# Kernel optimization log

Hardware: AMD Instinct MI355X
Metric: run time of the kernel (lower is better)

## Reference

```python
import jax, jax.numpy as jnp
import numpy as np

N = 50000      # nodes
E = 800000     # edges (avg degree 16)
IN = 128       # input feature dim
HID = 32       # per-head hidden dim
H = 4          # attention heads
C = 40         # num classes
SLOPE = 0.2    # leaky relu negative slope


def setup_inputs() -> dict:
    key = jax.random.key(0)
    ks = jax.random.split(key, 14)
    s = 0.05
    inputs = jax.random.normal(ks[0], (N, IN), jnp.float32)
    target = jax.random.normal(ks[1], (N, IN), jnp.float32)
    lamb = jax.random.uniform(ks[2], (1,), jnp.float32)
    src = jax.random.randint(ks[3], (E,), 0, N, jnp.int32)
    dst = jax.random.randint(ks[4], (E,), 0, N, jnp.int32)
    W0 = jax.random.normal(ks[5], (IN, H * HID), jnp.float32) * s
    al0 = jax.random.normal(ks[6], (H, HID), jnp.float32) * s
    ar0 = jax.random.normal(ks[7], (H, HID), jnp.float32) * s
    W1 = jax.random.normal(ks[8], (H * HID, H * HID), jnp.float32) * s
    al1 = jax.random.normal(ks[9], (H, HID), jnp.float32) * s
    ar1 = jax.random.normal(ks[10], (H, HID), jnp.float32) * s
    Wout = jax.random.normal(ks[11], (H * HID, C), jnp.float32) * s
    bout = jnp.zeros((C,), jnp.float32)
    return dict(inputs=inputs, target=target, lamb=lamb,
                W0=W0, al0=al0, ar0=ar0, W1=W1, al1=al1, ar1=ar1,
                Wout=Wout, bout=bout, src=src, dst=dst)


def gat_conv(h, W, al, ar, src, dst, residual):
    # h: [N, in_dim]; W: [in_dim, H*HID]; al/ar: [H, HID]
    feat = (h @ W).reshape(N, H, HID)                  # [N,H,D]
    el = jnp.einsum('nhd,hd->nh', feat, al)            # [N,H]
    er = jnp.einsum('nhd,hd->nh', feat, ar)            # [N,H]
    e = jax.nn.leaky_relu(el[src] + er[dst], SLOPE)    # [E,H]
    # edge softmax over incoming edges of each dst node
    emax = jax.ops.segment_max(e, dst, num_segments=N)  # [N,H]
    ee = jnp.exp(e - emax[dst])                          # [E,H]
    denom = jax.ops.segment_sum(ee, dst, num_segments=N)
    a = ee / denom[dst]                                  # [E,H]
    msg = feat[src] * a[:, :, None]                      # [E,H,D]
    out = jax.ops.segment_sum(msg, dst, num_segments=N)  # [N,H,D]
    if residual:
        out = out + h.reshape(N, H, HID)  # identity residual (in == H*HID)
    return jax.nn.elu(out)


def reference(inputs, target, lamb, W0, al0, ar0, W1, al1, ar1, Wout, bout, src, dst):
    def path(x):
        h = gat_conv(x, W0, al0, ar0, src, dst, residual=False).reshape(N, H * HID)
        h = gat_conv(h, W1, al1, ar1, src, dst, residual=True).reshape(N, H * HID)
        return h

    h = path(inputs)
    h2 = path(target)
    lam = lamb[0]
    h = lam * h + (1.0 - lam) * h2   # mixup_hidden=True
    logits = h @ Wout + bout
    return (h, logits)
```

## Files before the change

### kernel.cpp

```cpp
#include <hip/hip_runtime.h>
#include <hip/hip_bf16.h>
#include <cstddef>

#define GN 50000
#define GE 800000
#define GH 4
#define GD 32
#define SLOPE 0.2f
#define LOG2E 1.4426950408889634f

typedef unsigned short ushort_t;
typedef unsigned int uint_t;
using short8 = __attribute__((ext_vector_type(8))) short;
using float4v = __attribute__((ext_vector_type(4))) float;

__device__ __forceinline__ ushort_t f2bf(float f) {
    union { float f; uint_t u; } v; v.f = f;
    uint_t r = v.u + 0x7fff + ((v.u >> 16) & 1);
    return (ushort_t)(r >> 16);
}
__device__ __forceinline__ float bflo(uint_t u) { return __uint_as_float(u << 16); }
__device__ __forceinline__ float bfhi(uint_t u) { return __uint_as_float(u & 0xffff0000u); }
__device__ __forceinline__ float bfu(ushort_t u) { return __uint_as_float((uint_t)u << 16); }

__device__ __forceinline__ uint_t cvt_pk_bf16(float lo, float hi) {
    uint_t r;
    asm("v_cvt_pk_bf16_f32 %0, %1, %2" : "=v"(r) : "v"(lo), "v"(hi));
    return r;
}

#if __has_builtin(__builtin_amdgcn_exp2f)
#define EXP2F(x) __builtin_amdgcn_exp2f(x)
#else
#define EXP2F(x) exp2f(x)
#endif

__global__ void k_hist(const int* __restrict__ dst, int* __restrict__ deg, int E) {
    int i = blockIdx.x * 256 + threadIdx.x;
    if (i < E) atomicAdd(&deg[dst[i]], 1);
}

__global__ void k_scan1(const int* __restrict__ deg, int* __restrict__ row_ptr,
                        int* __restrict__ partials, int n) {
    __shared__ int s[256];
    int t = threadIdx.x;
    int i = blockIdx.x * 256 + t;
    int v = (i < n) ? deg[i] : 0;
    s[t] = v;
    __syncthreads();
    for (int off = 1; off < 256; off <<= 1) {
        int add = (t >= off) ? s[t - off] : 0;
        __syncthreads();
        s[t] += add;
        __syncthreads();
    }
    if (i < n) row_ptr[i] = s[t] - v;
    if (t == 255) partials[blockIdx.x] = s[255];
}

__global__ void k_scan2(int* __restrict__ partials, int nb) {
    __shared__ int s[256];
    int t = threadIdx.x;
    int v = (t < nb) ? partials[t] : 0;
    s[t] = v;
    __syncthreads();
    for (int off = 1; off < 256; off <<= 1) {
        int add = (t >= off) ? s[t - off] : 0;
        __syncthreads();
        s[t] += add;
        __syncthreads();
    }
    if (t < nb) partials[t] = s[t] - v;
}

__global__ void k_scan3(int* __restrict__ row_ptr, int* __restrict__ wpos,
                        const int* __restrict__ partials, int n, int E) {
    int i = blockIdx.x * 256 + threadIdx.x;
    if (i < n) {
        int rp = row_ptr[i] + partials[i >> 8];
        row_ptr[i] = rp;
        wpos[i] = rp;
        if (i == 0) row_ptr[n] = E;
    }
}

__global__ void k_fill(const int* __restrict__ src, const int* __restrict__ dst,
                       int* __restrict__ wpos, int* __restrict__ csr_src, int E) {
    int i = blockIdx.x * 256 + threadIdx.x;
    if (i < E) {
        int p = atomicAdd(&wpos[dst[i]], 1);
        csr_src[p] = src[i];
    }
}

__global__ void k_cvt_w(const float* __restrict__ W0, const float* __restrict__ W1,
                        ushort_t* __restrict__ wbt) {
    int t = blockIdx.x * 256 + threadIdx.x;
    int m = t >> 14;
    int o = t & 16383;
    int n = o >> 7, k = o & 127;
    const float* W = m ? W1 : W0;
    wbt[t] = f2bf(W[k * 128 + n]);
}

__global__ void k_cvt_wout(const float* __restrict__ Wout, ushort_t* __restrict__ wb) {
    int t = blockIdx.x * 256 + threadIdx.x;
    if (t >= 48 * 128) return;
    int n = t >> 7, k = t & 127;
    float w = (n < 40) ? Wout[k * 40 + n] : 0.f;
    ushort_t h = f2bf(w);
    float r = w - bfu(h);
    wb[t] = h;
    wb[48 * 128 + t] = f2bf(r);
}

__device__ __forceinline__ void lr_epilogue(const float4v acc[2][8],
                                            const float* __restrict__ al,
                                            const float* __restrict__ ar,
                                            float* __restrict__ el,
                                            float* __restrict__ er,
                                            int r0, int quad, int col, int M) {
#pragma unroll
    for (int rt = 0; rt < 2; rt++) {
#pragma unroll
        for (int h = 0; h < 4; h++) {
            float alv0 = al[h * 32 + col], alv1 = al[h * 32 + 16 + col];
            float arv0 = ar[h * 32 + col], arv1 = ar[h * 32 + 16 + col];
            float pl[4], pr[4];
#pragma unroll
            for (int r = 0; r < 4; r++) {
                pl[r] = acc[rt][2 * h][r] * alv0 + acc[rt][2 * h + 1][r] * alv1;
                pr[r] = acc[rt][2 * h][r] * arv0 + acc[rt][2 * h + 1][r] * arv1;
            }
#pragma unroll
            for (int m = 1; m < 16; m <<= 1) {
#pragma unroll
                for (int r = 0; r < 4; r++) {
                    pl[r] += __shfl_xor(pl[r], m, 64);
                    pr[r] += __shfl_xor(pr[r], m, 64);
                }
            }
            if (col == h) {
#pragma unroll
                for (int r = 0; r < 4; r++) {
                    int row = r0 + rt * 16 + quad * 4 + r;
                    if (row < M) el[row * 4 + h] = pl[r] * LOG2E;
                }
            }
            if (col == 8 + h) {
#pragma unroll
                for (int r = 0; r < 4; r++) {
                    int row = r0 + rt * 16 + quad * 4 + r;
                    if (row < M) er[row * 4 + h] = pr[r] * LOG2E;
                }
            }
        }
    }
}

__device__ __forceinline__ void store_c_bf16(ushort_t* __restrict__ Cb,
                                             const float4v acc[2][8],
                                             int r0, int quad, int col, int M) {
#pragma unroll
    for (int rt = 0; rt < 2; rt++)
#pragma unroll
        for (int nt = 0; nt < 8; nt++) {
            int rb = r0 + rt * 16 + quad * 4;
            int c = nt * 16 + col;
            uint_t p01 = cvt_pk_bf16(acc[rt][nt][0], acc[rt][nt][1]);
            uint_t p23 = cvt_pk_bf16(acc[rt][nt][2], acc[rt][nt][3]);
            if (rb + 0 < M) Cb[(size_t)(rb + 0) * 128 + c] = (ushort_t)p01;
            if (rb + 1 < M) Cb[(size_t)(rb + 1) * 128 + c] = (ushort_t)(p01 >> 16);
            if (rb + 2 < M) Cb[(size_t)(rb + 2) * 128 + c] = (ushort_t)p23;
            if (rb + 3 < M) Cb[(size_t)(rb + 3) * 128 + c] = (ushort_t)(p23 >> 16);
        }
}

__global__ __launch_bounds__(256) void gemm_mfma32(const float* __restrict__ A0,
                                                   const float* __restrict__ A1,
                                                   const ushort_t* __restrict__ WbT,
                                                   const float* __restrict__ al,
                                                   const float* __restrict__ ar,
                                                   ushort_t* __restrict__ Cb,
                                                   float* __restrict__ el,
                                                   float* __restrict__ er, int M) {
    __shared__ ushort_t Bs[128][136];
    int tid = threadIdx.x;
    for (int i = tid; i < 128 * 16; i += 256) {
        int n = i >> 4;
        int kc = (i & 15) << 3;
        *(short8*)&Bs[n][kc] = *(const short8*)&WbT[n * 128 + kc];
    }
    __syncthreads();
    int wid = tid >> 6, lane = tid & 63;
    int r0 = blockIdx.x * 128 + wid * 32;
    int col = lane & 15, quad = lane >> 4;
    float4v acc[2][8];
#pragma unroll
    for (int rt = 0; rt < 2; rt++)
#pragma unroll
        for (int t = 0; t < 8; t++) acc[rt][t] = (float4v){0.f, 0.f, 0.f, 0.f};
    int ar_[2] = {r0 + col, r0 + 16 + col};
    const float* Ap[2];
#pragma unroll
    for (int rt = 0; rt < 2; rt++) {
        int a = ar_[rt];
        Ap[rt] = (a < M) ? ((a < GN) ? (A0 + (size_t)a * 128)
                                     : (A1 + (size_t)(a - GN) * 128)) : nullptr;
    }
#pragma unroll
    for (int ks = 0; ks < 4; ks++) {
        short8 af[2];
#pragma unroll
        for (int rt = 0; rt < 2; rt++) {
            af[rt] = (short8){};
            if (Ap[rt]) {
                float4 v0 = *(const float4*)&Ap[rt][ks * 32 + quad * 8];
                float4 v1 = *(const float4*)&Ap[rt][ks * 32 + quad * 8 + 4];
                union { short8 s; uint_t u[4]; } cv;
                cv.u[0] = cvt_pk_bf16(v0.x, v0.y);
                cv.u[1] = cvt_pk_bf16(v0.z, v0.w);
                cv.u[2] = cvt_pk_bf16(v1.x, v1.y);
                cv.u[3] = cvt_pk_bf16(v1.z, v1.w);
                af[rt] = cv.s;
            }
        }
#pragma unroll
        for (int nt = 0; nt < 8; nt++) {
            short8 bf = *(const short8*)&Bs[nt * 16 + col][ks * 32 + quad * 8];
            acc[0][nt] = __builtin_amdgcn_mfma_f32_16x16x32_bf16(af[0], bf, acc[0][nt], 0, 0, 0);
            acc[1][nt] = __builtin_amdgcn_mfma_f32_16x16x32_bf16(af[1], bf, acc[1][nt], 0, 0, 0);
        }
    }
    store_c_bf16(Cb, acc, r0, quad, col, M);
    lr_epilogue(acc, al, ar, el, er, r0, quad, col, M);
}

__global__ __launch_bounds__(256) void gemm_mfma(const ushort_t* __restrict__ A,
                                                 const ushort_t* __restrict__ WbT,
                                                 const float* __restrict__ al,
                                                 const float* __restrict__ ar,
                                                 ushort_t* __restrict__ Cb,
                                                 float* __restrict__ el,
                                                 float* __restrict__ er, int M) {
    __shared__ ushort_t Bs[128][136];
    int tid = threadIdx.x;
    for (int i = tid; i < 128 * 16; i += 256) {
        int n = i >> 4;
        int kc = (i & 15) << 3;
        *(short8*)&Bs[n][kc] = *(const short8*)&WbT[n * 128 + kc];
    }
    __syncthreads();
    int wid = tid >> 6, lane = tid & 63;
    int r0 = blockIdx.x * 128 + wid * 32;
    int col = lane & 15, quad = lane >> 4;
    float4v acc[2][8];
#pragma unroll
    for (int rt = 0; rt < 2; rt++)
#pragma unroll
        for (int t = 0; t < 8; t++) acc[rt][t] = (float4v){0.f, 0.f, 0.f, 0.f};
    int ar_[2] = {r0 + col, r0 + 16 + col};
#pragma unroll
    for (int ks = 0; ks < 4; ks++) {
        short8 af[2];
#pragma unroll
        for (int rt = 0; rt < 2; rt++) {
            af[rt] = (short8){};
            if (ar_[rt] < M) af[rt] = *(const short8*)&A[(size_t)ar_[rt] * 128 + ks * 32 + quad * 8];
        }
#pragma unroll
        for (int nt = 0; nt < 8; nt++) {
            short8 bf = *(const short8*)&Bs[nt * 16 + col][ks * 32 + quad * 8];
            acc[0][nt] = __builtin_amdgcn_mfma_f32_16x16x32_bf16(af[0], bf, acc[0][nt], 0, 0, 0);
            acc[1][nt] = __builtin_amdgcn_mfma_f32_16x16x32_bf16(af[1], bf, acc[1][nt], 0, 0, 0);
        }
    }
    store_c_bf16(Cb, acc, r0, quad, col, M);
    lr_epilogue(acc, al, ar, el, er, r0, quad, col, M);
}

__device__ __forceinline__ void agg_core(
    const ushort_t* __restrict__ featb, const float* __restrict__ el, float ern,
    const int* __restrict__ csr_src, int base, int deg, uint_t ebase, uint_t fbase,
    float& v0, float& v1, float& v2, float& v3) {
    float a0 = 0.f, a1 = 0.f, a2 = 0.f, a3 = 0.f, ss = 0.f;
    int i = 0;
    for (; i + 8 <= deg; i += 8) {
        int j = base + i;
        int s0 = csr_src[j + 0], s1 = csr_src[j + 1], s2 = csr_src[j + 2], s3 = csr_src[j + 3];
        int s4 = csr_src[j + 4], s5 = csr_src[j + 5], s6 = csr_src[j + 6], s7 = csr_src[j + 7];
        float e0 = el[ebase + (uint_t)s0 * 4u] + ern;
        float e1 = el[ebase + (uint_t)s1 * 4u] + ern;
        float e2 = el[ebase + (uint_t)s2 * 4u] + ern;
        float e3 = el[ebase + (uint_t)s3 * 4u] + ern;
        float e4 = el[ebase + (uint_t)s4 * 4u] + ern;
        float e5 = el[ebase + (uint_t)s5 * 4u] + ern;
        float e6 = el[ebase + (uint_t)s6 * 4u] + ern;
        float e7 = el[ebase + (uint_t)s7 * 4u] + ern;
        uint2 f0 = *(const uint2*)&featb[fbase + (uint_t)s0 * 128u];
        uint2 f1 = *(const uint2*)&featb[fbase + (uint_t)s1 * 128u];
        uint2 f2 = *(const uint2*)&featb[fbase + (uint_t)s2 * 128u];
        uint2 f3 = *(const uint2*)&featb[fbase + (uint_t)s3 * 128u];
        uint2 f4 = *(const uint2*)&featb[fbase + (uint_t)s4 * 128u];
        uint2 f5 = *(const uint2*)&featb[fbase + (uint_t)s5 * 128u];
        uint2 f6 = *(const uint2*)&featb[fbase + (uint_t)s6 * 128u];
        uint2 f7 = *(const uint2*)&featb[fbase + (uint_t)s7 * 128u];
        e0 = fmaxf(e0, SLOPE * e0);
        e1 = fmaxf(e1, SLOPE * e1);
        e2 = fmaxf(e2, SLOPE * e2);
        e3 = fmaxf(e3, SLOPE * e3);
        e4 = fmaxf(e4, SLOPE * e4);
        e5 = fmaxf(e5, SLOPE * e5);
        e6 = fmaxf(e6, SLOPE * e6);
        e7 = fmaxf(e7, SLOPE * e7);
        float w0 = EXP2F(e0), w1 = EXP2F(e1), w2 = EXP2F(e2), w3 = EXP2F(e3);
        float w4 = EXP2F(e4), w5 = EXP2F(e5), w6 = EXP2F(e6), w7 = EXP2F(e7);
        ss += ((w0 + w1) + (w2 + w3)) + ((w4 + w5) + (w6 + w7));
        a0 += w0 * bflo(f0.x) + w1 * bflo(f1.x) + w2 * bflo(f2.x) + w3 * bflo(f3.x) +
              w4 * bflo(f4.x) + w5 * bflo(f5.x) + w6 * bflo(f6.x) + w7 * bflo(f7.x);
        a1 += w0 * bfhi(f0.x) + w1 * bfhi(f1.x) + w2 * bfhi(f2.x) + w3 * bfhi(f3.x) +
              w4 * bfhi(f4.x) + w5 * bfhi(f5.x) + w6 * bfhi(f6.x) + w7 * bfhi(f7.x);
        a2 += w0 * bflo(f0.y) + w1 * bflo(f1.y) + w2 * bflo(f2.y) + w3 * bflo(f3.y) +
              w4 * bflo(f4.y) + w5 * bflo(f5.y) + w6 * bflo(f6.y) + w7 * bflo(f7.y);
        a3 += w0 * bfhi(f0.y) + w1 * bfhi(f1.y) + w2 * bfhi(f2.y) + w3 * bfhi(f3.y) +
              w4 * bfhi(f4.y) + w5 * bfhi(f5.y) + w6 * bfhi(f6.y) + w7 * bfhi(f7.y);
    }
    for (; i < deg; i++) {
        int j = base + i;
        int s = csr_src[j];
        float e = el[ebase + (uint_t)s * 4u] + ern;
        uint2 f = *(const uint2*)&featb[fbase + (uint_t)s * 128u];
        e = fmaxf(e, SLOPE * e);
        float w = EXP2F(e);
        ss += w;
        a0 += w * bflo(f.x);
        a1 += w * bfhi(f.x);
        a2 += w * bflo(f.y);
        a3 += w * bfhi(f.y);
    }
    float inv = (deg > 0) ? 1.f / ss : 0.f;
    v0 = a0 * inv; v1 = a1 * inv; v2 = a2 * inv; v3 = a3 * inv;
}

__global__ __launch_bounds__(256) void gat_agg_l1(
    const ushort_t* __restrict__ featb, const float* __restrict__ el,
    const float* __restrict__ er, const int* __restrict__ row_ptr,
    const int* __restrict__ csr_src, ushort_t* __restrict__ abuf) {
    int n = blockIdx.x * 4 + (threadIdx.x >> 6);
    if (n >= GN) return;
    int lane = threadIdx.x & 63;
    int half = lane >> 5;
    int q = lane & 31;
    int head = q >> 3, q4 = q << 2;
    uint_t ebase = (uint_t)(half * (GN * 4) + head);
    uint_t fbase = (uint_t)(half * (GN * 128) + q4);
    float ern = er[ebase + (uint_t)n * 4u];
    int base = row_ptr[n];
    int deg = row_ptr[n + 1] - base;
    float v0, v1, v2, v3;
    agg_core(featb, el, ern, csr_src, base, deg, ebase, fbase, v0, v1, v2, v3);
    v0 = v0 > 0.f ? v0 : __expf(v0) - 1.f;
    v1 = v1 > 0.f ? v1 : __expf(v1) - 1.f;
    v2 = v2 > 0.f ? v2 : __expf(v2) - 1.f;
    v3 = v3 > 0.f ? v3 : __expf(v3) - 1.f;
    size_t idx = ((size_t)n + (size_t)half * GN) * 128 + q4;
    uint2 o;
    o.x = cvt_pk_bf16(v0, v1);
    o.y = cvt_pk_bf16(v2, v3);
    *(uint2*)&abuf[idx] = o;
}

__global__ __launch_bounds__(256) void gat_agg_l2(
    const ushort_t* __restrict__ featb, const float* __restrict__ el,
    const float* __restrict__ er, const int* __restrict__ row_ptr,
    const int* __restrict__ csr_src, const ushort_t* __restrict__ resid,
    const float* __restrict__ lamb, float* __restrict__ outh) {
    int tid = threadIdx.x;
    int n = blockIdx.x * 4 + (tid >> 6);
    if (n >= GN) return;
    int lane = tid & 63;
    int half = lane >> 5;
    int q = lane & 31;
    int head = q >> 3, q4 = q << 2;
    uint_t ebase = (uint_t)(half * (GN * 4) + head);
    uint_t fbase = (uint_t)(half * (GN * 128) + q4);
    float ern = er[ebase + (uint_t)n * 4u];
    int base = row_ptr[n];
    int deg = row_ptr[n + 1] - base;
    float v0, v1, v2, v3;
    agg_core(featb, el, ern, csr_src, base, deg, ebase, fbase, v0, v1, v2, v3);
    size_t idx = ((size_t)n + (size_t)half * GN) * 128 + q4;
    ushort4 r = *(const ushort4*)&resid[idx];
    v0 += bfu(r.x); v1 += bfu(r.y); v2 += bfu(r.z); v3 += bfu(r.w);
    v0 = v0 > 0.f ? v0 : __expf(v0) - 1.f;
    v1 = v1 > 0.f ? v1 : __expf(v1) - 1.f;
    v2 = v2 > 0.f ? v2 : __expf(v2) - 1.f;
    v3 = v3 > 0.f ? v3 : __expf(v3) - 1.f;
    float p0 = __shfl_xor(v0, 32, 64);
    float p1 = __shfl_xor(v1, 32, 64);
    float p2 = __shfl_xor(v2, 32, 64);
    float p3 = __shfl_xor(v3, 32, 64);
    float lam = lamb[0];
    if (half == 0) {
        float m0 = lam * v0 + (1.f - lam) * p0;
        float m1 = lam * v1 + (1.f - lam) * p1;
        float m2 = lam * v2 + (1.f - lam) * p2;
        float m3 = lam * v3 + (1.f - lam) * p3;
        *(float4*)&outh[(size_t)n * 128 + q4] = make_float4(m0, m1, m2, m3);
    }
}

__global__ __launch_bounds__(256) void k_logits(const float* __restrict__ Hf,
                                                const ushort_t* __restrict__ Wb,
                                                const float* __restrict__ bout,
                                                float* __restrict__ outlog) {
    __shared__ ushort_t Bh[48][136];
    __shared__ ushort_t Bl[48][136];
    int tid = threadIdx.x;
    for (int i = tid; i < 48 * 16; i += 256) {
        int n = i >> 4;
        int kc = (i & 15) << 3;
        *(short8*)&Bh[n][kc] = *(const short8*)&Wb[n * 128 + kc];
        *(short8*)&Bl[n][kc] = *(const short8*)&Wb[48 * 128 + n * 128 + kc];
    }
    __syncthreads();
    int wid = tid >> 6, lane = tid & 63;
    int r0 = blockIdx.x * 128 + wid * 32;
    int col = lane & 15, quad = lane >> 4;
    float4v acc[2][3];
#pragma unroll
    for (int rt = 0; rt < 2; rt++)
#pragma unroll
        for (int nt = 0; nt < 3; nt++) acc[rt][nt] = (float4v){0.f, 0.f, 0.f, 0.f};
    int ar_[2] = {r0 + col, r0 + 16 + col};
#pragma unroll
    for (int ks = 0; ks < 4; ks++) {
        short8 ah[2], alo[2];
#pragma unroll
        for (int rt = 0; rt < 2; rt++) {
            ah[rt] = (short8){};
            alo[rt] = (short8){};
            if (ar_[rt] < GN) {
                const float* p = Hf + (size_t)ar_[rt] * 128 + ks * 32 + quad * 8;
                float4 x = *(const float4*)p;
                float4 y = *(const float4*)(p + 4);
                union { short8 s; uint_t u[4]; } ch, cl;
                ch.u[0] = cvt_pk_bf16(x.x, x.y);
                ch.u[1] = cvt_pk_bf16(x.z, x.w);
                ch.u[2] = cvt_pk_bf16(y.x, y.y);
                ch.u[3] = cvt_pk_bf16(y.z, y.w);
                cl.u[0] = cvt_pk_bf16(x.x - bflo(ch.u[0]), x.y - bfhi(ch.u[0]));
                cl.u[1] = cvt_pk_bf16(x.z - bflo(ch.u[1]), x.w - bfhi(ch.u[1]));
                cl.u[2] = cvt_pk_bf16(y.x - bflo(ch.u[2]), y.y - bfhi(ch.u[2]));
                cl.u[3] = cvt_pk_bf16(y.z - bflo(ch.u[3]), y.w - bfhi(ch.u[3]));
                ah[rt] = ch.s;
                alo[rt] = cl.s;
            }
        }
#pragma unroll
        for (int nt = 0; nt < 3; nt++) {
            short8 bh = *(const short8*)&Bh[nt * 16 + col][ks * 32 + quad * 8];
            short8 bl = *(const short8*)&Bl[nt * 16 + col][ks * 32 + quad * 8];
#pragma unroll
            for (int rt = 0; rt < 2; rt++) {
                acc[rt][nt] = __builtin_amdgcn_mfma_f32_16x16x32_bf16(ah[rt], bh, acc[rt][nt], 0, 0, 0);
                acc[rt][nt] = __builtin_amdgcn_mfma_f32_16x16x32_bf16(alo[rt], bh, acc[rt][nt], 0, 0, 0);
                acc[rt][nt] = __builtin_amdgcn_mfma_f32_16x16x32_bf16(ah[rt], bl, acc[rt][nt], 0, 0, 0);
            }
        }
    }
#pragma unroll
    for (int nt = 0; nt < 3; nt++) {
        int c = nt * 16 + col;
        if (c < 40) {
            float bv = bout[c];
#pragma unroll
            for (int rt = 0; rt < 2; rt++)
#pragma unroll
                for (int r = 0; r < 4; r++) {
                    int row = r0 + rt * 16 + quad * 4 + r;
                    if (row < GN) outlog[(size_t)row * 40 + c] = acc[rt][nt][r] + bv;
                }
        }
    }
}

extern "C" void kernel_launch(void* const* d_in, const int* in_sizes, int n_in,
                              void* d_out, int out_size, void* d_ws, size_t ws_size,
                              hipStream_t stream) {
    const float* inputs = (const float*)d_in[0];
    const float* target = (const float*)d_in[1];
    const float* lamb   = (const float*)d_in[2];
    const float* W0     = (const float*)d_in[3];
    const float* al0    = (const float*)d_in[4];
    const float* ar0    = (const float*)d_in[5];
    const float* W1     = (const float*)d_in[6];
    const float* al1    = (const float*)d_in[7];
    const float* ar1    = (const float*)d_in[8];
    const float* Wout   = (const float*)d_in[9];
    const float* bout   = (const float*)d_in[10];
    const int*   src    = (const int*)d_in[11];
    const int*   dst    = (const int*)d_in[12];

    float* out = (float*)d_out;
    float* outh = out;
    float* outlog = out + (size_t)GN * 128;

    const int NP = 2 * GN;
    ushort_t* featb = (ushort_t*)d_ws;
    ushort_t* abuf  = featb + (size_t)NP * 128;
    float* el = (float*)(abuf + (size_t)NP * 128);
    float* er = el + (size_t)NP * GH;
    ushort_t* wbt = (ushort_t*)(er + (size_t)NP * GH);
    int* row_ptr  = (int*)(wbt + 2 * 128 * 128);
    int* wpos     = row_ptr + (GN + 1);
    int* csr_src  = wpos + GN;
    int* partials = csr_src + GE + 16;
    ushort_t* woutb = (ushort_t*)(partials + 256);

    const int nb = (GN + 255) / 256;
    const int eb = (GE + 255) / 256;
    const int gblocks = (NP + 127) / 128;
    const int aggblocks = (GN + 3) / 4;
    const int lblocks = (GN + 127) / 128;

    hipMemsetAsync(wpos, 0, GN * sizeof(int), stream);
    k_hist<<<eb, 256, 0, stream>>>(dst, wpos, GE);
    k_scan1<<<nb, 256, 0, stream>>>(wpos, row_ptr, partials, GN);
    k_scan2<<<1, 256, 0, stream>>>(partials, nb);
    k_scan3<<<nb, 256, 0, stream>>>(row_ptr, wpos, partials, GN, GE);
    k_fill<<<eb, 256, 0, stream>>>(src, dst, wpos, csr_src, GE);

    k_cvt_w<<<128, 256, 0, stream>>>(W0, W1, wbt);
    k_cvt_wout<<<24, 256, 0, stream>>>(Wout, woutb);

    gemm_mfma32<<<gblocks, 256, 0, stream>>>(inputs, target, wbt, al0, ar0,
                                             featb, el, er, NP);
    gat_agg_l1<<<aggblocks, 256, 0, stream>>>(featb, el, er, row_ptr, csr_src, abuf);

    gemm_mfma<<<gblocks, 256, 0, stream>>>(abuf, wbt + 128 * 128, al1, ar1,
                                           featb, el, er, NP);
    gat_agg_l2<<<aggblocks, 256, 0, stream>>>(featb, el, er, row_ptr, csr_src,
                                              abuf, lamb, outh);

    k_logits<<<lblocks, 256, 0, stream>>>(outh, woutb, bout, outlog);
}
```

Before: 417.3 us.

## Share edge softmax weights via ds_swizzle and prefetch next CSR indices

In the aggregation core, each lane in a group of eight now computes one edge's attention weight (one el load and one exp2) and broadcasts it to the other lanes with ds_swizzle. Before, every lane computed all eight. The next batch of CSR source indices is loaded during the current iteration to hide index-load latency. The node index is made wave-uniform with readfirstlane so row_ptr and csr_src reads can become scalar loads. This adds swizzle traffic through LDS hardware and a loop-carried register set.

```diff
diff --git a/kernel.cpp b/kernel.cpp
--- a/kernel.cpp
+++ b/kernel.cpp
@@ -34,6 +34,8 @@
 #else
 #define EXP2F(x) exp2f(x)
 #endif
+
+#define SWZ_B(v, imm) __uint_as_float((uint_t)__builtin_amdgcn_ds_swizzle((int)__float_as_uint(v), (imm)))
 
 __global__ void k_hist(const int* __restrict__ dst, int* __restrict__ deg, int E) {
     int i = blockIdx.x * 256 + threadIdx.x;
@@ -281,55 +283,73 @@
 
 __device__ __forceinline__ void agg_core(
     const ushort_t* __restrict__ featb, const float* __restrict__ el, float ern,
-    const int* __restrict__ csr_src, int base, int deg, uint_t ebase, uint_t fbase,
-    float& v0, float& v1, float& v2, float& v3) {
+    const int* __restrict__ csr_src, int base, int deg, uint_t ebase, uint_t fofs,
+    int lane, float& v0, float& v1, float& v2, float& v3) {
     float a0 = 0.f, a1 = 0.f, a2 = 0.f, a3 = 0.f, ss = 0.f;
-    int i = 0;
-    for (; i + 8 <= deg; i += 8) {
-        int j = base + i;
-        int s0 = csr_src[j + 0], s1 = csr_src[j + 1], s2 = csr_src[j + 2], s3 = csr_src[j + 3];
-        int s4 = csr_src[j + 4], s5 = csr_src[j + 5], s6 = csr_src[j + 6], s7 = csr_src[j + 7];
-        float e0 = el[ebase + (uint_t)s0 * 4u] + ern;
-        float e1 = el[ebase + (uint_t)s1 * 4u] + ern;
-        float e2 = el[ebase + (uint_t)s2 * 4u] + ern;
-        float e3 = el[ebase + (uint_t)s3 * 4u] + ern;
-        float e4 = el[ebase + (uint_t)s4 * 4u] + ern;
-        float e5 = el[ebase + (uint_t)s5 * 4u] + ern;
-        float e6 = el[ebase + (uint_t)s6 * 4u] + ern;
-        float e7 = el[ebase + (uint_t)s7 * 4u] + ern;
-        uint2 f0 = *(const uint2*)&featb[fbase + (uint_t)s0 * 128u];
-        uint2 f1 = *(const uint2*)&featb[fbase + (uint_t)s1 * 128u];
-        uint2 f2 = *(const uint2*)&featb[fbase + (uint_t)s2 * 128u];
-        uint2 f3 = *(const uint2*)&featb[fbase + (uint_t)s3 * 128u];
-        uint2 f4 = *(const uint2*)&featb[fbase + (uint_t)s4 * 128u];
-        uint2 f5 = *(const uint2*)&featb[fbase + (uint_t)s5 * 128u];
-        uint2 f6 = *(const uint2*)&featb[fbase + (uint_t)s6 * 128u];
-        uint2 f7 = *(const uint2*)&featb[fbase + (uint_t)s7 * 128u];
-        e0 = fmaxf(e0, SLOPE * e0);
-        e1 = fmaxf(e1, SLOPE * e1);
-        e2 = fmaxf(e2, SLOPE * e2);
-        e3 = fmaxf(e3, SLOPE * e3);
-        e4 = fmaxf(e4, SLOPE * e4);
-        e5 = fmaxf(e5, SLOPE * e5);
-        e6 = fmaxf(e6, SLOPE * e6);
-        e7 = fmaxf(e7, SLOPE * e7);
-        float w0 = EXP2F(e0), w1 = EXP2F(e1), w2 = EXP2F(e2), w3 = EXP2F(e3);
-        float w4 = EXP2F(e4), w5 = EXP2F(e5), w6 = EXP2F(e6), w7 = EXP2F(e7);
-        ss += ((w0 + w1) + (w2 + w3)) + ((w4 + w5) + (w6 + w7));
-        a0 += w0 * bflo(f0.x) + w1 * bflo(f1.x) + w2 * bflo(f2.x) + w3 * bflo(f3.x) +
-              w4 * bflo(f4.x) + w5 * bflo(f5.x) + w6 * bflo(f6.x) + w7 * bflo(f7.x);
-        a1 += w0 * bfhi(f0.x) + w1 * bfhi(f1.x) + w2 * bfhi(f2.x) + w3 * bfhi(f3.x) +
-              w4 * bfhi(f4.x) + w5 * bfhi(f5.x) + w6 * bfhi(f6.x) + w7 * bfhi(f7.x);
-        a2 += w0 * bflo(f0.y) + w1 * bflo(f1.y) + w2 * bflo(f2.y) + w3 * bflo(f3.y) +
-              w4 * bflo(f4.y) + w5 * bflo(f5.y) + w6 * bflo(f6.y) + w7 * bflo(f7.y);
-        a3 += w0 * bfhi(f0.y) + w1 * bfhi(f1.y) + w2 * bfhi(f2.y) + w3 * bfhi(f3.y) +
-              w4 * bfhi(f4.y) + w5 * bfhi(f5.y) + w6 * bfhi(f6.y) + w7 * bfhi(f7.y);
-    }
-    for (; i < deg; i++) {
-        int j = base + i;
-        int s = csr_src[j];
+    int nmain = deg & ~7;
+    int lk = lane & 7;
+    if (nmain) {
+        int jb = base;
+        int s0 = csr_src[jb + 0], s1 = csr_src[jb + 1], s2 = csr_src[jb + 2], s3 = csr_src[jb + 3];
+        int s4 = csr_src[jb + 4], s5 = csr_src[jb + 5], s6 = csr_src[jb + 6], s7 = csr_src[jb + 7];
+        int sown = csr_src[jb + lk];
+        int i = 0;
+        for (;;) {
+            const ushort_t* p0 = featb + (uint_t)s0 * 128u;
+            const ushort_t* p1 = featb + (uint_t)s1 * 128u;
+            const ushort_t* p2 = featb + (uint_t)s2 * 128u;
+            const ushort_t* p3 = featb + (uint_t)s3 * 128u;
+            const ushort_t* p4 = featb + (uint_t)s4 * 128u;
+            const ushort_t* p5 = featb + (uint_t)s5 * 128u;
+            const ushort_t* p6 = featb + (uint_t)s6 * 128u;
+            const ushort_t* p7 = featb + (uint_t)s7 * 128u;
+            uint2 f0 = *(const uint2*)&p0[fofs];
+            uint2 f1 = *(const uint2*)&p1[fofs];
+            uint2 f2 = *(const uint2*)&p2[fofs];
+            uint2 f3 = *(const uint2*)&p3[fofs];
+            uint2 f4 = *(const uint2*)&p4[fofs];
+            uint2 f5 = *(const uint2*)&p5[fofs];
+            uint2 f6 = *(const uint2*)&p6[fofs];
+            uint2 f7 = *(const uint2*)&p7[fofs];
+            float e = el[ebase + (uint_t)sown * 4u] + ern;
+            bool more = (i + 8) < nmain;
+            int t0 = 0, t1 = 0, t2 = 0, t3 = 0, t4 = 0, t5 = 0, t6 = 0, t7 = 0, town = 0;
+            if (more) {
+                int nj = jb + 8;
+                t0 = csr_src[nj + 0]; t1 = csr_src[nj + 1]; t2 = csr_src[nj + 2]; t3 = csr_src[nj + 3];
+                t4 = csr_src[nj + 4]; t5 = csr_src[nj + 5]; t6 = csr_src[nj + 6]; t7 = csr_src[nj + 7];
+                town = csr_src[nj + lk];
+            }
+            e = fmaxf(e, SLOPE * e);
+            float wown = EXP2F(e);
+            float w0 = SWZ_B(wown, 0x018);
+            float w1 = SWZ_B(wown, 0x038);
+            float w2 = SWZ_B(wown, 0x058);
+            float w3 = SWZ_B(wown, 0x078);
+            float w4 = SWZ_B(wown, 0x098);
+            float w5 = SWZ_B(wown, 0x0B8);
+            float w6 = SWZ_B(wown, 0x0D8);
+            float w7 = SWZ_B(wown, 0x0F8);
+            ss += ((w0 + w1) + (w2 + w3)) + ((w4 + w5) + (w6 + w7));
+            a0 += w0 * bflo(f0.x) + w1 * bflo(f1.x) + w2 * bflo(f2.x) + w3 * bflo(f3.x) +
+                  w4 * bflo(f4.x) + w5 * bflo(f5.x) + w6 * bflo(f6.x) + w7 * bflo(f7.x);
+            a1 += w0 * bfhi(f0.x) + w1 * bfhi(f1.x) + w2 * bfhi(f2.x) + w3 * bfhi(f3.x) +
+                  w4 * bfhi(f4.x) + w5 * bfhi(f5.x) + w6 * bfhi(f6.x) + w7 * bfhi(f7.x);
+            a2 += w0 * bflo(f0.y) + w1 * bflo(f1.y) + w2 * bflo(f2.y) + w3 * bflo(f3.y) +
+                  w4 * bflo(f4.y) + w5 * bflo(f5.y) + w6 * bflo(f6.y) + w7 * bflo(f7.y);
+            a3 += w0 * bfhi(f0.y) + w1 * bfhi(f1.y) + w2 * bfhi(f2.y) + w3 * bfhi(f3.y) +
+                  w4 * bfhi(f4.y) + w5 * bfhi(f5.y) + w6 * bfhi(f6.y) + w7 * bfhi(f7.y);
+            if (!more) break;
+            i += 8; jb += 8;
+            s0 = t0; s1 = t1; s2 = t2; s3 = t3; s4 = t4; s5 = t5; s6 = t6; s7 = t7;
+            sown = town;
+        }
+    }
+    for (int i = nmain; i < deg; i++) {
+        int s = csr_src[base + i];
         float e = el[ebase + (uint_t)s * 4u] + ern;
-        uint2 f = *(const uint2*)&featb[fbase + (uint_t)s * 128u];
+        const ushort_t* p = featb + (uint_t)s * 128u;
+        uint2 f = *(const uint2*)&p[fofs];
         e = fmaxf(e, SLOPE * e);
         float w = EXP2F(e);
         ss += w;
@@ -346,19 +366,19 @@
     const ushort_t* __restrict__ featb, const float* __restrict__ el,
     const float* __restrict__ er, const int* __restrict__ row_ptr,
     const int* __restrict__ csr_src, ushort_t* __restrict__ abuf) {
-    int n = blockIdx.x * 4 + (threadIdx.x >> 6);
+    int n = __builtin_amdgcn_readfirstlane(blockIdx.x * 4 + (threadIdx.x >> 6));
     if (n >= GN) return;
     int lane = threadIdx.x & 63;
     int half = lane >> 5;
     int q = lane & 31;
-    int head = q >> 3, q4 = q << 2;
+    int head = (lane >> 3) & 3, q4 = q << 2;
     uint_t ebase = (uint_t)(half * (GN * 4) + head);
-    uint_t fbase = (uint_t)(half * (GN * 128) + q4);
+    uint_t fofs = (uint_t)(half * (GN * 128) + q4);
     float ern = er[ebase + (uint_t)n * 4u];
     int base = row_ptr[n];
     int deg = row_ptr[n + 1] - base;
     float v0, v1, v2, v3;
-    agg_core(featb, el, ern, csr_src, base, deg, ebase, fbase, v0, v1, v2, v3);
+    agg_core(featb, el, ern, csr_src, base, deg, ebase, fofs, lane, v0, v1, v2, v3);
     v0 = v0 > 0.f ? v0 : __expf(v0) - 1.f;
     v1 = v1 > 0.f ? v1 : __expf(v1) - 1.f;
     v2 = v2 > 0.f ? v2 : __expf(v2) - 1.f;
@@ -376,19 +396,19 @@
     const int* __restrict__ csr_src, const ushort_t* __restrict__ resid,
     const float* __restrict__ lamb, float* __restrict__ outh) {
     int tid = threadIdx.x;
-    int n = blockIdx.x * 4 + (tid >> 6);
+    int n = __builtin_amdgcn_readfirstlane(blockIdx.x * 4 + (tid >> 6));
     if (n >= GN) return;
     int lane = tid & 63;
     int half = lane >> 5;
     int q = lane & 31;
-    int head = q >> 3, q4 = q << 2;
+    int head = (lane >> 3) & 3, q4 = q << 2;
     uint_t ebase = (uint_t)(half * (GN * 4) + head);
-    uint_t fbase = (uint_t)(half * (GN * 128) + q4);
+    uint_t fofs = (uint_t)(half * (GN * 128) + q4);
     float ern = er[ebase + (uint_t)n * 4u];
     int base = row_ptr[n];
     int deg = row_ptr[n + 1] - base;
     float v0, v1, v2, v3;
-    agg_core(featb, el, ern, csr_src, base, deg, ebase, fbase, v0, v1, v2, v3);
+    agg_core(featb, el, ern, csr_src, base, deg, ebase, fofs, lane, v0, v1, v2, v3);
     size_t idx = ((size_t)n + (size_t)half * GN) * 128 + q4;
     ushort4 r = *(const ushort4*)&resid[idx];
     v0 += bfu(r.x); v1 += bfu(r.y); v2 += bfu(r.z); v3 += bfu(r.w);
```

Result: no change. 415.2 us (-0.5%).
